# Kernel tuning notes

Hardware: AMD Instinct MI355X
Metric: run time of the kernel (lower is better)

Reference implementation:

```python
import jax, jax.numpy as jnp
import numpy as np

LN_EPS = 1e-5

def _layer_norm(x, gamma, beta):
    mu = x.mean(-1, keepdims=True)
    var = ((x - mu) ** 2).mean(-1, keepdims=True)
    return (x - mu) * jax.lax.rsqrt(var + LN_EPS) * gamma + beta

def _neg_sq_dist(q, p):
    # q: [B,Qtot,H], p: [B,N,H] -> [B,Qtot,N]
    return -jnp.sum((q[:, :, None, :] - p[:, None, :, :]) ** 2, axis=-1)

def setup_inputs() -> dict:
    key = jax.random.key(0)
    k1, k2 = jax.random.split(key)
    B, N, K, Q, H = 512, 10, 5, 5, 256
    Qtot = N * Q  # na_rate = 0
    return {
        "support": jax.random.normal(k1, (B, N * K, H), dtype=jnp.float32),
        "query": jax.random.normal(k2, (B, Qtot, H), dtype=jnp.float32),
        "ln_gamma": jnp.ones((H,), dtype=jnp.float32),
        "ln_beta": jnp.zeros((H,), dtype=jnp.float32),
        "N": N,
        "K": K,
        "Q": Q,
    }

def reference(support, query, ln_gamma, ln_beta, N, K, Q):
    B, _, H = support.shape
    s = _layer_norm(support, ln_gamma, ln_beta).reshape(B, N, K, H)
    q = _layer_norm(query, ln_gamma, ln_beta)          # [B, Qtot, H]
    Qtot = q.shape[1]

    M = s.mean(axis=2)                                  # [B, N, H] mean prototype
    # --- __rectify__ ---
    Xq = _neg_sq_dist(q, M)                             # [B, Qtot, N]
    Cq = jnp.argmax(Xq, axis=-1)                        # [B, Qtot] nearest proto
    # padded support memory [B, N, K+Qtot, H]
    Xp = jnp.pad(s, ((0, 0), (0, 0), (0, Qtot), (0, 0)))
    b_idx = jnp.arange(B)[:, None]
    q_idx = jnp.arange(Qtot)[None, :]
    # each (b,q) writes a unique slot q+K -> no collisions
    Xp = Xp.at[b_idx, Cq, q_idx + K].set(q)
    counts = jax.nn.one_hot(Cq, N, dtype=jnp.float32).sum(axis=1)  # [B, N]
    Xp_size = (K + counts)[:, :, None]                  # [B, N, 1]

    scores = jnp.einsum("bnsh,bnh->bns", Xp, M)[..., None]  # [B,N,S,1]
    M_cos = jax.nn.softmax(scores, axis=1)              # softmax over N dim
    proto = (M_cos * Xp).sum(axis=-2) / Xp_size          # [B, N, H]
    # --- logits ---
    logits = _neg_sq_dist(q, proto)                     # [B, Qtot, N]
    minn = logits.min(axis=-1, keepdims=True)
    logits = jnp.concatenate([logits, minn - 1.0], axis=-1)  # [B, Qtot, N+1]
    pred = jnp.argmax(logits.reshape(-1, N + 1), axis=1)
    return logits, pred
```

## Files before the change

### kernel.cpp

```cpp
#include <hip/hip_runtime.h>
#include <math.h>

#define LN_EPS 1e-5f

constexpr int Nn  = 10;
constexpr int Kk  = 5;
constexpr int Hh  = 256;
constexpr int QT  = 50;
constexpr int NP1 = 11;

template<int CTRL, int RM>
__device__ __forceinline__ float dpp_term(float x) {
    return __int_as_float(__builtin_amdgcn_update_dpp(
        0, __float_as_int(x), CTRL, RM, 0xf, true));
}
__device__ __forceinline__ float sum16_bcast(float v) {
    v += dpp_term<0xB1,  0xf>(v);
    v += dpp_term<0x4E,  0xf>(v);
    v += dpp_term<0x124, 0xf>(v);
    v += dpp_term<0x128, 0xf>(v);
    return v;
}
__device__ __forceinline__ float sum64_lane63(float v) {
    v += dpp_term<0x111, 0xf>(v);
    v += dpp_term<0x112, 0xf>(v);
    v += dpp_term<0x114, 0xf>(v);
    v += dpp_term<0x118, 0xf>(v);
    v += dpp_term<0x142, 0xa>(v);
    v += dpp_term<0x143, 0xc>(v);
    return v;
}
__device__ __forceinline__ float rdlane(float v, int l) {
    return __int_as_float(__builtin_amdgcn_readlane(__float_as_int(v), l));
}
__device__ __forceinline__ float wave64_sum_bcast(float v) {
    return rdlane(sum64_lane63(v), 63);
}

__device__ __forceinline__ float dot16_ilp4(const float y16[16],
                                            const float* __restrict__ rowbase,
                                            int sub) {
    float p0, p1, p2, p3;
    {
        const float4 v = *reinterpret_cast<const float4*>(rowbase + 0 * 64 + sub * 4);
        p0 = y16[0] * v.x; p0 = fmaf(y16[1], v.y, p0);
        p0 = fmaf(y16[2], v.z, p0); p0 = fmaf(y16[3], v.w, p0);
    }
    {
        const float4 v = *reinterpret_cast<const float4*>(rowbase + 1 * 64 + sub * 4);
        p1 = y16[4] * v.x; p1 = fmaf(y16[5], v.y, p1);
        p1 = fmaf(y16[6], v.z, p1); p1 = fmaf(y16[7], v.w, p1);
    }
    {
        const float4 v = *reinterpret_cast<const float4*>(rowbase + 2 * 64 + sub * 4);
        p2 = y16[8] * v.x; p2 = fmaf(y16[9], v.y, p2);
        p2 = fmaf(y16[10], v.z, p2); p2 = fmaf(y16[11], v.w, p2);
    }
    {
        const float4 v = *reinterpret_cast<const float4*>(rowbase + 3 * 64 + sub * 4);
        p3 = y16[12] * v.x; p3 = fmaf(y16[13], v.y, p3);
        p3 = fmaf(y16[14], v.z, p3); p3 = fmaf(y16[15], v.w, p3);
    }
    return (p0 + p1) + (p2 + p3);
}

__global__ __launch_bounds__(1024, 8) void proto_rectify_fused(
    const float* __restrict__ support, const float* __restrict__ query,
    const float* __restrict__ gamma,   const float* __restrict__ beta,
    float* __restrict__ out, int B)
{
    const int b    = blockIdx.x;
    const int tid  = threadIdx.x;
    const int lane = tid & 63;
    const int wave = tid >> 6;
    const int grp  = tid >> 4;
    const int sub  = tid & 15;

    __shared__ float qy_s[QT][Hh];
    __shared__ float MP_s[Nn][Hh];
    __shared__ float nM_s[Nn], np_s[Nn];
    __shared__ float ny_s[QT];
    __shared__ float score_s[Nn * Kk];
    __shared__ float wsup_s[Nn * Kk];
    __shared__ float wq_s[QT];
    __shared__ int   cq_s[QT];
    __shared__ float sstat_s[Nn * Kk][2];
    __shared__ int   cnt_s[Nn];

    const float* supB = support + (size_t)b * (Nn * Kk * Hh);
    const float* qryB = query   + (size_t)b * (QT * Hh);

    if (tid < Nn) cnt_s[tid] = 0;

    const float4 g4 = *reinterpret_cast<const float4*>(gamma + lane * 4);
    const float4 b4 = *reinterpret_cast<const float4*>(beta  + lane * 4);
    if (wave < Nn) {
        const int n = wave;
        const float* rows = supB + (size_t)n * Kk * Hh;

        float y[Kk][4];
#pragma unroll
        for (int k = 0; k < Kk; ++k) {
            const float4 x = *reinterpret_cast<const float4*>(rows + k * Hh + lane * 4);
            float s  = x.x + x.y + x.z + x.w;
            float ss = x.x * x.x + x.y * x.y + x.z * x.z + x.w * x.w;
            s  = wave64_sum_bcast(s);
            ss = wave64_sum_bcast(ss);
            const float mu   = s * (1.0f / (float)Hh);
            const float rstd = rsqrtf(ss * (1.0f / (float)Hh) - mu * mu + LN_EPS);
            if (lane == 0) { sstat_s[n * Kk + k][0] = mu; sstat_s[n * Kk + k][1] = rstd; }
            y[k][0] = (x.x - mu) * rstd * g4.x + b4.x;
            y[k][1] = (x.y - mu) * rstd * g4.y + b4.y;
            y[k][2] = (x.z - mu) * rstd * g4.z + b4.z;
            y[k][3] = (x.w - mu) * rstd * g4.w + b4.w;
        }
        float Mv[4];
#pragma unroll
        for (int i = 0; i < 4; ++i)
            Mv[i] = (y[0][i] + y[1][i] + y[2][i] + y[3][i] + y[4][i]) / 5.0f;
        *reinterpret_cast<float4*>(&MP_s[n][lane * 4]) =
            make_float4(Mv[0], Mv[1], Mv[2], Mv[3]);

        float pm = Mv[0] * Mv[0];
        pm = fmaf(Mv[1], Mv[1], pm); pm = fmaf(Mv[2], Mv[2], pm); pm = fmaf(Mv[3], Mv[3], pm);
        pm = sum64_lane63(pm);
        if (lane == 63) nM_s[n] = pm;

#pragma unroll
        for (int k = 0; k < Kk; ++k) {
            float p = y[k][0] * Mv[0];
            p = fmaf(y[k][1], Mv[1], p); p = fmaf(y[k][2], Mv[2], p); p = fmaf(y[k][3], Mv[3], p);
            p = sum64_lane63(p);
            if (lane == 63) score_s[n * Kk + k] = p;
        }
    } else {
        for (int r = wave - 10; r < QT; r += 6) {
            const float4 x = *reinterpret_cast<const float4*>(
                qryB + (size_t)r * Hh + lane * 4);
            float s  = x.x + x.y + x.z + x.w;
            float ss = fmaf(x.x, x.x, fmaf(x.y, x.y, fmaf(x.z, x.z, x.w * x.w)));
            s  = wave64_sum_bcast(s);
            ss = wave64_sum_bcast(ss);
            const float mu   = s * (1.0f / (float)Hh);
            const float rstd = rsqrtf(ss * (1.0f / (float)Hh) - mu * mu + LN_EPS);
            float y0 = (x.x - mu) * rstd * g4.x + b4.x;
            float y1 = (x.y - mu) * rstd * g4.y + b4.y;
            float y2 = (x.z - mu) * rstd * g4.z + b4.z;
            float y3 = (x.w - mu) * rstd * g4.w + b4.w;
            *reinterpret_cast<float4*>(&qy_s[r][lane * 4]) =
                make_float4(y0, y1, y2, y3);
            float ny = fmaf(y0, y0, fmaf(y1, y1, fmaf(y2, y2, y3 * y3)));
            ny = sum64_lane63(ny);
            if (lane == 63) ny_s[r] = ny;
        }
    }
    __syncthreads();

    if (grp < QT) {
        const int q = grp;
        const float nmv = (lane < Nn) ? nM_s[lane] : 0.f;
        float y16[16];
#pragma unroll
        for (int c = 0; c < 4; ++c) {
            const float4 v = *reinterpret_cast<const float4*>(&qy_s[q][c * 64 + sub * 4]);
            y16[c * 4 + 0] = v.x; y16[c * 4 + 1] = v.y;
            y16[c * 4 + 2] = v.z; y16[c * 4 + 3] = v.w;
        }
        float bestd = INFINITY, bestdot = 0.f;
        int bestn = 0;
#pragma unroll
        for (int n = 0; n < Nn; ++n) {
            float p = dot16_ilp4(y16, &MP_s[n][0], sub);
            p = sum16_bcast(p);
            const float d = rdlane(nmv, n) - 2.0f * p;
            if (d < bestd) { bestd = d; bestn = n; bestdot = p; }
        }
        if (sub == 0) {
            const float sc  = bestdot;
            const float mx  = fmaxf(sc, 0.f);
            const float e   = expf(sc - mx);
            const float den = e + (float)(Nn - 1) * expf(-mx);
            wq_s[q] = e / den;
            cq_s[q] = bestn;
            atomicAdd(&cnt_s[bestn], 1);
        }
    } else if (grp >= 56 && grp < 56 + Kk && sub == 0) {
        const int k = grp - 56;
        float mx = -INFINITY;
#pragma unroll
        for (int n = 0; n < Nn; ++n) mx = fmaxf(mx, score_s[n * Kk + k]);
        float e[Nn]; float den = 0.f;
#pragma unroll
        for (int n = 0; n < Nn; ++n) { e[n] = expf(score_s[n * Kk + k] - mx); den += e[n]; }
#pragma unroll
        for (int n = 0; n < Nn; ++n) wsup_s[n * Kk + k] = e[n] / den;
    }
    __syncthreads();

    if (wave < Nn) {
        const int n = wave;
        const float* rows = supB + (size_t)n * Kk * Hh;

        float acc[4] = {0.f, 0.f, 0.f, 0.f};
#pragma unroll
        for (int k = 0; k < Kk; ++k) {
            const float w    = wsup_s[n * Kk + k];
            const float mu   = sstat_s[n * Kk + k][0];
            const float rstd = sstat_s[n * Kk + k][1];
            const float4 x = *reinterpret_cast<const float4*>(rows + k * Hh + lane * 4);
            acc[0] = fmaf(w, (x.x - mu) * rstd * g4.x + b4.x, acc[0]);
            acc[1] = fmaf(w, (x.y - mu) * rstd * g4.y + b4.y, acc[1]);
            acc[2] = fmaf(w, (x.z - mu) * rstd * g4.z + b4.z, acc[2]);
            acc[3] = fmaf(w, (x.w - mu) * rstd * g4.w + b4.w, acc[3]);
        }
        int myc = -1; float myw = 0.f;
        if (lane < QT) { myc = cq_s[lane]; myw = wq_s[lane]; }
        unsigned long long mask = __ballot(lane < QT && myc == n);
        while (mask) {
            const int q = __ffsll(mask) - 1;
            mask &= mask - 1;
            const float w = rdlane(myw, q);
            const float4 yv = *reinterpret_cast<const float4*>(&qy_s[q][lane * 4]);
            acc[0] = fmaf(w, yv.x, acc[0]);
            acc[1] = fmaf(w, yv.y, acc[1]);
            acc[2] = fmaf(w, yv.z, acc[2]);
            acc[3] = fmaf(w, yv.w, acc[3]);
        }
        const float inv = 1.0f / (float)(Kk + cnt_s[n]);
        float pv[4];
#pragma unroll
        for (int i = 0; i < 4; ++i) pv[i] = acc[i] * inv;
        *reinterpret_cast<float4*>(&MP_s[n][lane * 4]) =
            make_float4(pv[0], pv[1], pv[2], pv[3]);
        float pp = pv[0] * pv[0];
        pp = fmaf(pv[1], pv[1], pp); pp = fmaf(pv[2], pv[2], pp); pp = fmaf(pv[3], pv[3], pp);
        pp = sum64_lane63(pp);
        if (lane == 63) np_s[n] = pp;
    }
    __syncthreads();

    if (grp < QT) {
        const int q = grp;
        const float npv = (lane < Nn) ? np_s[lane] : 0.f;
        float y16[16];
#pragma unroll
        for (int c = 0; c < 4; ++c) {
            const float4 v = *reinterpret_cast<const float4*>(&qy_s[q][c * 64 + sub * 4]);
            y16[c * 4 + 0] = v.x; y16[c * 4 + 1] = v.y;
            y16[c * 4 + 2] = v.z; y16[c * 4 + 3] = v.w;
        }
        const float ny = ny_s[q];

        float mine = 0.f, maxd = -INFINITY, bestd = INFINITY;
        int bestn = 0;
#pragma unroll
        for (int n = 0; n < Nn; ++n) {
            float p = dot16_ilp4(y16, &MP_s[n][0], sub);
            p = sum16_bcast(p);
            const float d = ny + rdlane(npv, n) - 2.0f * p;
            if (sub == n) mine = d;
            maxd = fmaxf(maxd, d);
            if (d < bestd) { bestd = d; bestn = n; }
        }
        float* o = out + ((size_t)b * QT + q) * NP1;
        if (sub < Nn)       o[sub] = -mine;
        else if (sub == Nn) o[Nn]  = -maxd - 1.0f;
        else if (sub == Nn + 1)
            out[(size_t)B * QT * NP1 + (size_t)b * QT + q] = (float)bestn;
    }
}

extern "C" void kernel_launch(void* const* d_in, const int* in_sizes, int n_in,
                              void* d_out, int out_size, void* d_ws, size_t ws_size,
                              hipStream_t stream) {
    const float* support = (const float*)d_in[0];
    const float* query   = (const float*)d_in[1];
    const float* gamma   = (const float*)d_in[2];
    const float* beta    = (const float*)d_in[3];
    float* out = (float*)d_out;

    const int B = in_sizes[0] / (Nn * Kk * Hh);
    proto_rectify_fused<<<B, 1024, 0, stream>>>(support, query, gamma, beta, out, B);
}
```

Measured before the change: 25.74 us.

## Process two queries per 16-lane group and prefetch query rows in LayerNorm

Each 16-lane group now handles two queries, so every prototype row loaded from LDS feeds two dot products. This halves the number of active groups and interleaves two independent FMA chains. The query-norm computation moves from the LayerNorm phase into the first distance phase, and the LayerNorm loop software-prefetches the next row. The cost is more register pressure and less parallelism within each phase.

```diff
diff --git a/kernel.cpp b/kernel.cpp
--- a/kernel.cpp
+++ b/kernel.cpp
@@ -7,6 +7,7 @@
 constexpr int Kk  = 5;
 constexpr int Hh  = 256;
 constexpr int QT  = 50;
+constexpr int QH  = 25;
 constexpr int NP1 = 11;
 
 template<int CTRL, int RM>
@@ -35,33 +36,6 @@
 }
 __device__ __forceinline__ float wave64_sum_bcast(float v) {
     return rdlane(sum64_lane63(v), 63);
-}
-
-__device__ __forceinline__ float dot16_ilp4(const float y16[16],
-                                            const float* __restrict__ rowbase,
-                                            int sub) {
-    float p0, p1, p2, p3;
-    {
-        const float4 v = *reinterpret_cast<const float4*>(rowbase + 0 * 64 + sub * 4);
-        p0 = y16[0] * v.x; p0 = fmaf(y16[1], v.y, p0);
-        p0 = fmaf(y16[2], v.z, p0); p0 = fmaf(y16[3], v.w, p0);
-    }
-    {
-        const float4 v = *reinterpret_cast<const float4*>(rowbase + 1 * 64 + sub * 4);
-        p1 = y16[4] * v.x; p1 = fmaf(y16[5], v.y, p1);
-        p1 = fmaf(y16[6], v.z, p1); p1 = fmaf(y16[7], v.w, p1);
-    }
-    {
-        const float4 v = *reinterpret_cast<const float4*>(rowbase + 2 * 64 + sub * 4);
-        p2 = y16[8] * v.x; p2 = fmaf(y16[9], v.y, p2);
-        p2 = fmaf(y16[10], v.z, p2); p2 = fmaf(y16[11], v.w, p2);
-    }
-    {
-        const float4 v = *reinterpret_cast<const float4*>(rowbase + 3 * 64 + sub * 4);
-        p3 = y16[12] * v.x; p3 = fmaf(y16[13], v.y, p3);
-        p3 = fmaf(y16[14], v.z, p3); p3 = fmaf(y16[15], v.w, p3);
-    }
-    return (p0 + p1) + (p2 + p3);
 }
 
 __global__ __launch_bounds__(1024, 8) void proto_rectify_fused(
@@ -134,55 +108,102 @@
             if (lane == 63) score_s[n * Kk + k] = p;
         }
     } else {
-        for (int r = wave - 10; r < QT; r += 6) {
-            const float4 x = *reinterpret_cast<const float4*>(
-                qryB + (size_t)r * Hh + lane * 4);
+        int r = wave - 10;
+        float4 x = make_float4(0.f, 0.f, 0.f, 0.f);
+        if (r < QT) x = *reinterpret_cast<const float4*>(qryB + (size_t)r * Hh + lane * 4);
+        while (r < QT) {
+            const int rn = r + 6;
+            float4 xn = x;
+            if (rn < QT)
+                xn = *reinterpret_cast<const float4*>(qryB + (size_t)rn * Hh + lane * 4);
             float s  = x.x + x.y + x.z + x.w;
             float ss = fmaf(x.x, x.x, fmaf(x.y, x.y, fmaf(x.z, x.z, x.w * x.w)));
             s  = wave64_sum_bcast(s);
             ss = wave64_sum_bcast(ss);
             const float mu   = s * (1.0f / (float)Hh);
             const float rstd = rsqrtf(ss * (1.0f / (float)Hh) - mu * mu + LN_EPS);
-            float y0 = (x.x - mu) * rstd * g4.x + b4.x;
-            float y1 = (x.y - mu) * rstd * g4.y + b4.y;
-            float y2 = (x.z - mu) * rstd * g4.z + b4.z;
-            float y3 = (x.w - mu) * rstd * g4.w + b4.w;
-            *reinterpret_cast<float4*>(&qy_s[r][lane * 4]) =
-                make_float4(y0, y1, y2, y3);
-            float ny = fmaf(y0, y0, fmaf(y1, y1, fmaf(y2, y2, y3 * y3)));
-            ny = sum64_lane63(ny);
-            if (lane == 63) ny_s[r] = ny;
+            *reinterpret_cast<float4*>(&qy_s[r][lane * 4]) = make_float4(
+                (x.x - mu) * rstd * g4.x + b4.x,
+                (x.y - mu) * rstd * g4.y + b4.y,
+                (x.z - mu) * rstd * g4.z + b4.z,
+                (x.w - mu) * rstd * g4.w + b4.w);
+            x = xn; r = rn;
         }
     }
     __syncthreads();
 
-    if (grp < QT) {
-        const int q = grp;
+    if (grp < QH) {
+        const int q0 = grp, q1 = grp + QH;
         const float nmv = (lane < Nn) ? nM_s[lane] : 0.f;
-        float y16[16];
+        float ya[16], yb[16];
 #pragma unroll
         for (int c = 0; c < 4; ++c) {
-            const float4 v = *reinterpret_cast<const float4*>(&qy_s[q][c * 64 + sub * 4]);
-            y16[c * 4 + 0] = v.x; y16[c * 4 + 1] = v.y;
-            y16[c * 4 + 2] = v.z; y16[c * 4 + 3] = v.w;
-        }
-        float bestd = INFINITY, bestdot = 0.f;
-        int bestn = 0;
+            const float4 va = *reinterpret_cast<const float4*>(&qy_s[q0][c * 64 + sub * 4]);
+            ya[c * 4 + 0] = va.x; ya[c * 4 + 1] = va.y;
+            ya[c * 4 + 2] = va.z; ya[c * 4 + 3] = va.w;
+            const float4 vb = *reinterpret_cast<const float4*>(&qy_s[q1][c * 64 + sub * 4]);
+            yb[c * 4 + 0] = vb.x; yb[c * 4 + 1] = vb.y;
+            yb[c * 4 + 2] = vb.z; yb[c * 4 + 3] = vb.w;
+        }
+        {
+            float a0 = 0.f, a1 = 0.f, b0 = 0.f, b1 = 0.f;
+#pragma unroll
+            for (int j = 0; j < 8; ++j) {
+                a0 = fmaf(ya[j], ya[j], a0);
+                a1 = fmaf(ya[j + 8], ya[j + 8], a1);
+                b0 = fmaf(yb[j], yb[j], b0);
+                b1 = fmaf(yb[j + 8], yb[j + 8], b1);
+            }
+            const float nya = sum16_bcast(a0 + a1);
+            const float nyb = sum16_bcast(b0 + b1);
+            if (sub == 0) { ny_s[q0] = nya; ny_s[q1] = nyb; }
+        }
+        float bestdA = INFINITY, bestdotA = 0.f; int bestnA = 0;
+        float bestdB = INFINITY, bestdotB = 0.f; int bestnB = 0;
 #pragma unroll
         for (int n = 0; n < Nn; ++n) {
-            float p = dot16_ilp4(y16, &MP_s[n][0], sub);
-            p = sum16_bcast(p);
-            const float d = rdlane(nmv, n) - 2.0f * p;
-            if (d < bestd) { bestd = d; bestn = n; bestdot = p; }
+            const float4 m0 = *reinterpret_cast<const float4*>(&MP_s[n][0 * 64 + sub * 4]);
+            const float4 m1 = *reinterpret_cast<const float4*>(&MP_s[n][1 * 64 + sub * 4]);
+            const float4 m2 = *reinterpret_cast<const float4*>(&MP_s[n][2 * 64 + sub * 4]);
+            const float4 m3 = *reinterpret_cast<const float4*>(&MP_s[n][3 * 64 + sub * 4]);
+            float pa = ya[0] * m0.x;  float pb = yb[0] * m0.x;
+            pa = fmaf(ya[1],  m0.y, pa); pb = fmaf(yb[1],  m0.y, pb);
+            pa = fmaf(ya[2],  m0.z, pa); pb = fmaf(yb[2],  m0.z, pb);
+            pa = fmaf(ya[3],  m0.w, pa); pb = fmaf(yb[3],  m0.w, pb);
+            pa = fmaf(ya[4],  m1.x, pa); pb = fmaf(yb[4],  m1.x, pb);
+            pa = fmaf(ya[5],  m1.y, pa); pb = fmaf(yb[5],  m1.y, pb);
+            pa = fmaf(ya[6],  m1.z, pa); pb = fmaf(yb[6],  m1.z, pb);
+            pa = fmaf(ya[7],  m1.w, pa); pb = fmaf(yb[7],  m1.w, pb);
+            pa = fmaf(ya[8],  m2.x, pa); pb = fmaf(yb[8],  m2.x, pb);
+            pa = fmaf(ya[9],  m2.y, pa); pb = fmaf(yb[9],  m2.y, pb);
+            pa = fmaf(ya[10], m2.z, pa); pb = fmaf(yb[10], m2.z, pb);
+            pa = fmaf(ya[11], m2.w, pa); pb = fmaf(yb[11], m2.w, pb);
+            pa = fmaf(ya[12], m3.x, pa); pb = fmaf(yb[12], m3.x, pb);
+            pa = fmaf(ya[13], m3.y, pa); pb = fmaf(yb[13], m3.y, pb);
+            pa = fmaf(ya[14], m3.z, pa); pb = fmaf(yb[14], m3.z, pb);
+            pa = fmaf(ya[15], m3.w, pa); pb = fmaf(yb[15], m3.w, pb);
+            pa = sum16_bcast(pa);        pb = sum16_bcast(pb);
+            const float nm = rdlane(nmv, n);
+            const float da = nm - 2.0f * pa;
+            const float db = nm - 2.0f * pb;
+            if (da < bestdA) { bestdA = da; bestnA = n; bestdotA = pa; }
+            if (db < bestdB) { bestdB = db; bestnB = n; bestdotB = pb; }
         }
         if (sub == 0) {
-            const float sc  = bestdot;
-            const float mx  = fmaxf(sc, 0.f);
-            const float e   = expf(sc - mx);
-            const float den = e + (float)(Nn - 1) * expf(-mx);
-            wq_s[q] = e / den;
-            cq_s[q] = bestn;
-            atomicAdd(&cnt_s[bestn], 1);
+            {
+                const float mx  = fmaxf(bestdotA, 0.f);
+                const float e   = expf(bestdotA - mx);
+                const float den = e + (float)(Nn - 1) * expf(-mx);
+                wq_s[q0] = e / den;  cq_s[q0] = bestnA;
+                atomicAdd(&cnt_s[bestnA], 1);
+            }
+            {
+                const float mx  = fmaxf(bestdotB, 0.f);
+                const float e   = expf(bestdotB - mx);
+                const float den = e + (float)(Nn - 1) * expf(-mx);
+                wq_s[q1] = e / den;  cq_s[q1] = bestnB;
+                atomicAdd(&cnt_s[bestnB], 1);
+            }
         }
     } else if (grp >= 56 && grp < 56 + Kk && sub == 0) {
         const int k = grp - 56;
@@ -239,34 +260,64 @@
     }
     __syncthreads();
 
-    if (grp < QT) {
-        const int q = grp;
+    if (grp < QH) {
+        const int q0 = grp, q1 = grp + QH;
         const float npv = (lane < Nn) ? np_s[lane] : 0.f;
-        float y16[16];
+        float ya[16], yb[16];
 #pragma unroll
         for (int c = 0; c < 4; ++c) {
-            const float4 v = *reinterpret_cast<const float4*>(&qy_s[q][c * 64 + sub * 4]);
-            y16[c * 4 + 0] = v.x; y16[c * 4 + 1] = v.y;
-            y16[c * 4 + 2] = v.z; y16[c * 4 + 3] = v.w;
-        }
-        const float ny = ny_s[q];
-
-        float mine = 0.f, maxd = -INFINITY, bestd = INFINITY;
-        int bestn = 0;
+            const float4 va = *reinterpret_cast<const float4*>(&qy_s[q0][c * 64 + sub * 4]);
+            ya[c * 4 + 0] = va.x; ya[c * 4 + 1] = va.y;
+            ya[c * 4 + 2] = va.z; ya[c * 4 + 3] = va.w;
+            const float4 vb = *reinterpret_cast<const float4*>(&qy_s[q1][c * 64 + sub * 4]);
+            yb[c * 4 + 0] = vb.x; yb[c * 4 + 1] = vb.y;
+            yb[c * 4 + 2] = vb.z; yb[c * 4 + 3] = vb.w;
+        }
+        const float nya = ny_s[q0], nyb = ny_s[q1];
+
+        float mineA = 0.f, maxdA = -INFINITY, bestdA = INFINITY; int bestnA = 0;
+        float mineB = 0.f, maxdB = -INFINITY, bestdB = INFINITY; int bestnB = 0;
 #pragma unroll
         for (int n = 0; n < Nn; ++n) {
-            float p = dot16_ilp4(y16, &MP_s[n][0], sub);
-            p = sum16_bcast(p);
-            const float d = ny + rdlane(npv, n) - 2.0f * p;
-            if (sub == n) mine = d;
-            maxd = fmaxf(maxd, d);
-            if (d < bestd) { bestd = d; bestn = n; }
-        }
-        float* o = out + ((size_t)b * QT + q) * NP1;
-        if (sub < Nn)       o[sub] = -mine;
-        else if (sub == Nn) o[Nn]  = -maxd - 1.0f;
-        else if (sub == Nn + 1)
-            out[(size_t)B * QT * NP1 + (size_t)b * QT + q] = (float)bestn;
+            const float4 m0 = *reinterpret_cast<const float4*>(&MP_s[n][0 * 64 + sub * 4]);
+            const float4 m1 = *reinterpret_cast<const float4*>(&MP_s[n][1 * 64 + sub * 4]);
+            const float4 m2 = *reinterpret_cast<const float4*>(&MP_s[n][2 * 64 + sub * 4]);
+            const float4 m3 = *reinterpret_cast<const float4*>(&MP_s[n][3 * 64 + sub * 4]);
+            float pa = ya[0] * m0.x;  float pb = yb[0] * m0.x;
+            pa = fmaf(ya[1],  m0.y, pa); pb = fmaf(yb[1],  m0.y, pb);
+            pa = fmaf(ya[2],  m0.z, pa); pb = fmaf(yb[2],  m0.z, pb);
+            pa = fmaf(ya[3],  m0.w, pa); pb = fmaf(yb[3],  m0.w, pb);
+            pa = fmaf(ya[4],  m1.x, pa); pb = fmaf(yb[4],  m1.x, pb);
+            pa = fmaf(ya[5],  m1.y, pa); pb = fmaf(yb[5],  m1.y, pb);
+            pa = fmaf(ya[6],  m1.z, pa); pb = fmaf(yb[6],  m1.z, pb);
+            pa = fmaf(ya[7],  m1.w, pa); pb = fmaf(yb[7],  m1.w, pb);
+            pa = fmaf(ya[8],  m2.x, pa); pb = fmaf(yb[8],  m2.x, pb);
+            pa = fmaf(ya[9],  m2.y, pa); pb = fmaf(yb[9],  m2.y, pb);
+            pa = fmaf(ya[10], m2.z, pa); pb = fmaf(yb[10], m2.z, pb);
+            pa = fmaf(ya[11], m2.w, pa); pb = fmaf(yb[11], m2.w, pb);
+            pa = fmaf(ya[12], m3.x, pa); pb = fmaf(yb[12], m3.x, pb);
+            pa = fmaf(ya[13], m3.y, pa); pb = fmaf(yb[13], m3.y, pb);
+            pa = fmaf(ya[14], m3.z, pa); pb = fmaf(yb[14], m3.z, pb);
+            pa = fmaf(ya[15], m3.w, pa); pb = fmaf(yb[15], m3.w, pb);
+            pa = sum16_bcast(pa);        pb = sum16_bcast(pb);
+            const float np = rdlane(npv, n);
+            const float da = nya + np - 2.0f * pa;
+            const float db = nyb + np - 2.0f * pb;
+            if (sub == n) { mineA = da; mineB = db; }
+            maxdA = fmaxf(maxdA, da);
+            maxdB = fmaxf(maxdB, db);
+            if (da < bestdA) { bestdA = da; bestnA = n; }
+            if (db < bestdB) { bestdB = db; bestnB = n; }
+        }
+        if (sub == Nn) { mineA = -maxdA - 1.0f; mineB = -maxdB - 1.0f; }
+        else           { mineA = -mineA;        mineB = -mineB; }
+        float* o0 = out + ((size_t)b * QT + q0) * NP1;
+        float* o1 = out + ((size_t)b * QT + q1) * NP1;
+        if (sub <= Nn) { o0[sub] = mineA; o1[sub] = mineB; }
+        if (sub == Nn + 1) {
+            out[(size_t)B * QT * NP1 + (size_t)b * QT + q0] = (float)bestnA;
+            out[(size_t)B * QT * NP1 + (size_t)b * QT + q1] = (float)bestnB;
+        }
     }
 }
 
```

Result: slower. 42.44 us (+64.9%).
